# Performance work log

Hardware: AMD Instinct MI355X
Metric: run time of the kernel (lower is better)

## Reference

```python
import jax, jax.numpy as jnp
import numpy as np

N_HEADS = 8
WINDOW = 7

def _conv1x1(x, W, b):
    # x: [B,H,W,C]; 1x1 conv == per-pixel matmul
    return jnp.einsum('bhwc,cd->bhwd', x, W) + b

def _to_heads(t, nh):
    # [B,H,W,C] -> channels-first reshape [B, nh, C//nh, H*W] (matches tf transpose+reshape)
    B, H, W, C = t.shape
    return jnp.transpose(t, (0, 3, 1, 2)).reshape(B, nh, C // nh, H * W)

def setup_inputs() -> dict:
    key = jax.random.key(0)
    ks = jax.random.split(key, 8)
    B, H, W, C = 2, 56, 56, 256
    x = jax.random.normal(ks[0], (B, H, W, C), dtype=jnp.float32)
    s = 1.0 / np.sqrt(C)
    Wq = jax.random.normal(ks[1], (C, C), dtype=jnp.float32) * s
    bq = jnp.zeros((C,), dtype=jnp.float32)
    Wk = jax.random.normal(ks[2], (C, C), dtype=jnp.float32) * s
    bk = jnp.zeros((C,), dtype=jnp.float32)
    Wv = jax.random.normal(ks[3], (C, C), dtype=jnp.float32) * s
    bv = jnp.zeros((C,), dtype=jnp.float32)
    # original initializes gamma to 0 (output == x); use small nonzero so the
    # attention path is observable in outputs/grads
    gamma = jax.random.normal(ks[4], (1,), dtype=jnp.float32) * 0.1
    return {"x": x, "Wq": Wq, "bq": bq, "Wk": Wk, "bk": bk, "Wv": Wv, "bv": bv, "gamma": gamma}

def reference(x, Wq, bq, Wk, bk, Wv, bv, gamma):
    B, H, W, C = x.shape
    p = WINDOW // 2
    xp = jnp.pad(x, ((0, 0), (p, p), (p, p), (0, 0)), mode='reflect')  # [B,Hp,Wp,C]
    q = _to_heads(_conv1x1(x, Wq, bq), N_HEADS)    # [B,nh,dk,HW]
    k = _to_heads(_conv1x1(xp, Wk, bk), N_HEADS)   # [B,nh,dk,HpWp]
    v = _to_heads(_conv1x1(xp, Wv, bv), N_HEADS)   # [B,nh,dk,HpWp]
    energy = jnp.einsum('bhdq,bhdk->bhqk', q, k)   # [B,nh,HW,HpWp]
    attn = jax.nn.softmax(energy, axis=-1)
    out = jnp.einsum('bhdk,bhqk->bhdq', v, attn)   # [B,nh,dk,HW]
    out = out.reshape(B, C, H, W).transpose(0, 2, 3, 1)
    return gamma * out + x
```

## Files before the change

kernel.cpp:

```cpp
#include <hip/hip_runtime.h>

typedef unsigned short u16;
typedef float f32x4 __attribute__((ext_vector_type(4)));
typedef short bf16x8 __attribute__((ext_vector_type(8)));

__device__ __forceinline__ u16 f2bf(float f) {
    unsigned u = __float_as_uint(f);
    u = (u + 0x7FFFu + ((u >> 16) & 1u)) >> 16;
    return (u16)u;
}

#define LOG2E 1.4426950408889634f

#if __has_builtin(__builtin_amdgcn_exp2f)
__device__ __forceinline__ float exp2_fast(float x) { return __builtin_amdgcn_exp2f(x); }
#else
__device__ __forceinline__ float exp2_fast(float x) { return __expf(x * 0.6931471805599453f); }
#endif

__device__ __forceinline__ unsigned pack2bf(float a, float b) {
    unsigned ua = __float_as_uint(a) + 0x8000u;
    unsigned ub = __float_as_uint(b) + 0x8000u;
#if __has_builtin(__builtin_amdgcn_perm)
    return __builtin_amdgcn_perm(ub, ua, 0x07060302u);
#else
    return ((ua >> 16) & 0xFFFFu) | (ub & 0xFFFF0000u);
#endif
}

#if __has_builtin(__builtin_amdgcn_cvt_pk_bf16_f32)
typedef __bf16 bf2_t __attribute__((ext_vector_type(2)));
__device__ __forceinline__ unsigned cvtpk(float a, float b) {
    bf2_t r = __builtin_amdgcn_cvt_pk_bf16_f32(a, b);
    return __builtin_bit_cast(unsigned, r);
}
#else
__device__ __forceinline__ unsigned cvtpk(float a, float b) { return pack2bf(a, b); }
#endif

__device__ __forceinline__ bf16x8 bc8(uint4 u) { return __builtin_bit_cast(bf16x8, u); }

#if __has_builtin(__builtin_amdgcn_global_load_lds)
typedef const __attribute__((address_space(1))) void* as1cv;
typedef __attribute__((address_space(3))) void* as3v;
__device__ __forceinline__ void dma16(const void* g, void* lds_base, int lane) {
    __builtin_amdgcn_global_load_lds((as1cv)g, (as3v)lds_base, 16, 0, 0);
}
#else
__device__ __forceinline__ void dma16(const void* g, void* lds_base, int lane) {
    *(uint4*)((char*)lds_base + lane * 16) = *(const uint4*)g;
}
#endif

#define BB 2
#define HH 56
#define SQ 3136
#define CROWN 3584

#define WS_Q    0
#define WS_K    1605632
#define WS_V    3244032
#define WS_WT   4882432
#define WS_CB   5079040
#define WS_XB   5082624

__global__ __launch_bounds__(256) void prep_kernel(const float* __restrict__ x,
                                                   const float* __restrict__ Wq,
                                                   const float* __restrict__ Wk,
                                                   const float* __restrict__ Wv,
                                                   u16* __restrict__ wtf,
                                                   u16* __restrict__ kbf,
                                                   u16* __restrict__ vbf,
                                                   u16* __restrict__ crow,
                                                   u16* __restrict__ xbf) {
    __shared__ __align__(16) char SM[17408];
    int tid = threadIdx.x;
    int bid = blockIdx.x;

    if (bid < 48) {
        u16 (*T)[68] = (u16(*)[68])SM;
        int mode = bid >> 4, rem = bid & 15;
        int kx = (rem >> 2) * 64, dx = (rem & 3) * 64;
        const float* W = (mode == 0) ? Wq : ((mode == 1) ? Wk : Wv);
        float sc = (mode == 0) ? LOG2E : 1.0f;
        int r16 = tid >> 4, c4 = (tid & 15) * 4;
#pragma unroll
        for (int p = 0; p < 4; ++p) {
            int kr = p * 16 + r16;
            float4 f = *(const float4*)&W[(size_t)(kx + kr) * 256 + dx + c4];
            T[kr][c4 + 0] = f2bf(f.x * sc);
            T[kr][c4 + 1] = f2bf(f.y * sc);
            T[kr][c4 + 2] = f2bf(f.z * sc);
            T[kr][c4 + 3] = f2bf(f.w * sc);
        }
        __syncthreads();
        int l16 = tid & 15, nt_loc = (tid >> 4) & 3, quad = (tid >> 6) & 3;
#pragma unroll
        for (int s_loc = 0; s_loc < 2; ++s_loc) {
            int k0 = s_loc * 32 + quad * 8;
            int d_loc = nt_loc * 16 + l16;
            u16 tmp[8];
#pragma unroll
            for (int j = 0; j < 8; ++j) tmp[j] = T[k0 + j][d_loc];
            int d = dx + d_loc;
            int nz = d >> 7, ntg = (d >> 4) & 7;
            int s = (kx >> 5) + s_loc;
            int f = (nz * 8 + s) * 8 + ntg;
            int L = quad * 16 + l16;
            *(uint4*)&wtf[(size_t)mode * 65536 + (size_t)f * 512 + (size_t)L * 8] = *(uint4*)tmp;
        }
        uint4 z4 = (uint4){0, 0, 0, 0};
        if (mode == 0 && kx == 0 && dx == 0) {
            for (int i = tid; i < 4096; i += 256) {
                int bb = i >> 11, rem2 = i & 2047;
                int t = 196 + (rem2 >> 9), off = (rem2 & 511) * 8;
                *(uint4*)&kbf[(((size_t)(bb * 200 + t)) << 12) + off] = z4;
            }
        }
        if (mode == 1 && kx == 0 && dx == 0) {
            for (int i = tid; i < CROWN; i += 256) {
                u16 v = 0;
                if (i < SQ) {
                    int rr = i / 56, cc = i - rr * 56;
                    int mr = (((rr >= 1) && (rr <= 3)) || ((rr >= 52) && (rr <= 54))) ? 2 : 1;
                    int mc = (((cc >= 1) && (cc <= 3)) || ((cc >= 52) && (cc <= 54))) ? 2 : 1;
                    int prod = mr * mc;
                    v = (prod == 1) ? (u16)0x3F80 : ((prod == 2) ? (u16)0x4000 : (u16)0x4080);
                }
                crow[i] = v;
            }
        }
        if (mode == 2 && kx == 0 && dx == 0) {
            for (int i = tid; i < 4096; i += 256) {
                int bh = i >> 8, rem2 = i & 255;
                int rgp = 196 + (rem2 >> 6), off = (rem2 & 63) * 8;
                *(uint4*)&vbf[(((size_t)(bh * 200 + rgp)) << 9) + off] = z4;
            }
        }
    } else {
        float (*T)[256] = (float(*)[256])SM;
        int tile = bid - 48;
        int r = tid >> 4, c0 = (tid & 15) * 16;
        const float* src = x + ((size_t)tile * 16 + r) * 256 + c0;
#pragma unroll
        for (int k = 0; k < 4; ++k)
            *(float4*)&T[r][c0 + k * 4] = *(const float4*)&src[k * 4];
        __syncthreads();
#pragma unroll
        for (int e = 0; e < 2; ++e) {
            int g = tid + e * 256;
            int s = g >> 6, L = g & 63;
            const float* row = &T[L & 15][s * 32 + (L >> 4) * 8];
            uint4 pk = (uint4){pack2bf(row[0], row[1]), pack2bf(row[2], row[3]),
                               pack2bf(row[4], row[5]), pack2bf(row[6], row[7])};
            *(uint4*)&xbf[(size_t)tile * 4096 + (size_t)g * 8] = pk;
        }
    }
}

__global__ __launch_bounds__(256, 4) void proj_kernel(const u16* __restrict__ xbf,
                                                      const u16* __restrict__ wtf,
                                                      const float* __restrict__ bq,
                                                      const float* __restrict__ bk,
                                                      const float* __restrict__ bv,
                                                      u16* __restrict__ qbf,
                                                      u16* __restrict__ kbf,
                                                      u16* __restrict__ vbf) {
    int mode = blockIdx.y, nz = blockIdx.z;
    int mbase = blockIdx.x * 64;
    int tid = threadIdx.x;
    int wave = tid >> 6, lane = tid & 63, quad = (tid >> 4) & 3, l16 = tid & 15;
    const float* bias = (mode == 0) ? bq : ((mode == 1) ? bk : bv);
    float wsc = (mode == 0) ? LOG2E : 1.0f;
    const u16* wf = wtf + (size_t)mode * 65536 + (size_t)nz * 32768 + (size_t)lane * 8;
    const u16* xt = xbf + (((size_t)(mbase >> 4) + wave) << 12);

    f32x4 acc[8];
#pragma unroll
    for (int i = 0; i < 8; i++) acc[i] = (f32x4){0.f, 0.f, 0.f, 0.f};

#pragma unroll
    for (int s = 0; s < 8; ++s) {
        bf16x8 af = *(const bf16x8*)&xt[(s << 9) + lane * 8];
        if (mode == 2) {
#pragma unroll
            for (int nt = 0; nt < 8; nt++) {
                bf16x8 bfrag = *(const bf16x8*)&wf[(s * 8 + nt) * 512];
                acc[nt] = __builtin_amdgcn_mfma_f32_16x16x32_bf16(af, bfrag, acc[nt], 0, 0, 0);
            }
        } else {
#pragma unroll
            for (int nt = 0; nt < 8; nt++) {
                bf16x8 bfrag = *(const bf16x8*)&wf[(s * 8 + nt) * 512];
                acc[nt] = __builtin_amdgcn_mfma_f32_16x16x32_bf16(bfrag, af, acc[nt], 0, 0, 0);
            }
        }
    }

    if (mode == 2) {
        int b_ = (mbase >= SQ) ? 1 : 0;
        int kp0 = mbase - b_ * SQ + wave * 16 + quad * 4;
        int rg = (mbase - b_ * SQ + wave * 16) >> 4;
        float mult[4];
#pragma unroll
        for (int p = 0; p < 4; ++p) {
            int kp = kp0 + p;
            int rr = kp / 56, cc = kp - rr * 56;
            float mr = (((rr >= 1) && (rr <= 3)) || ((rr >= 52) && (rr <= 54))) ? 2.f : 1.f;
            float mc = (((cc >= 1) && (cc <= 3)) || ((cc >= 52) && (cc <= 54))) ? 2.f : 1.f;
            mult[p] = mr * mc;
        }
#pragma unroll
        for (int nt = 0; nt < 8; nt++) {
            int c = nz * 128 + nt * 16 + l16;
            float bvv = bias[c];
            int h_idx = nz * 4 + (nt >> 1);
            int L = (nt & 1) * 16 + l16 + ((quad >> 1) & 1) * 32;
            float va0 = (acc[nt][0] + bvv) * mult[0];
            float va1 = (acc[nt][1] + bvv) * mult[1];
            float va2 = (acc[nt][2] + bvv) * mult[2];
            float va3 = (acc[nt][3] + bvv) * mult[3];
            uint2 pk = (uint2){pack2bf(va0, va1), pack2bf(va2, va3)};
            *(uint2*)&vbf[(((size_t)((b_ * 8 + h_idx) * 200 + rg)) << 9) + L * 8 + (quad & 1) * 4] = pk;
        }
    } else {
        u16* outp = (mode == 0) ? qbf : kbf;
        int t = (mbase >> 4) + wave;
        int tt = (mode == 0) ? t : (t + (t >= 196 ? 4 : 0));
#pragma unroll
        for (int nt = 0; nt < 8; nt++) {
            int c0 = nz * 128 + nt * 16 + quad * 4;
            float4 b4 = *(const float4*)&bias[c0];
            float v0 = acc[nt][0] + b4.x * wsc;
            float v1 = acc[nt][1] + b4.y * wsc;
            float v2 = acc[nt][2] + b4.z * wsc;
            float v3 = acc[nt][3] + b4.w * wsc;
            int s_idx = nz * 4 + (nt >> 1);
            int Lrow = ((nt & 1) * 2 + (quad >> 1)) * 16 + l16;
            uint2 pk = (uint2){pack2bf(v0, v1), pack2bf(v2, v3)};
            *(uint2*)&outp[(((size_t)(tt * 8 + s_idx)) << 9) + Lrow * 8 + (quad & 1) * 4] = pk;
        }
    }
}

__global__ __launch_bounds__(256, 4) void attn_kernel(const u16* __restrict__ qb,
                                                      const u16* __restrict__ kb,
                                                      const u16* __restrict__ vtb,
                                                      const u16* __restrict__ crow,
                                                      const float* __restrict__ x,
                                                      const float* __restrict__ gammap,
                                                      float* __restrict__ out) {
    __shared__ __align__(16) u16 S[19968];

    int tid = threadIdx.x;
    int w = tid >> 6, lane = tid & 63, quad = lane >> 4, l16 = lane & 15;
    int bh = blockIdx.x;
    int b = bh >> 3, h = bh & 7;
    int qsub = blockIdx.y * 64;

    int qtile = b * 196 + blockIdx.y * 4;
    bf16x8 qf[4];
#pragma unroll
    for (int i = 0; i < 4; ++i)
        qf[i] = *(const bf16x8*)&qb[(((size_t)(qtile + i) * 8 + h) << 9) + lane * 8];

    const u16* kg = kb + ((size_t)(b * 200) << 12);
    const u16* vg = vtb + (((size_t)((b * 8 + h) * 200)) << 9);

    f32x4 o[4][2], lv[4];
#pragma unroll
    for (int i = 0; i < 4; ++i) {
        o[i][0] = (f32x4){0.f, 0.f, 0.f, 0.f};
        o[i][1] = (f32x4){0.f, 0.f, 0.f, 0.f};
        lv[i]   = (f32x4){0.f, 0.f, 0.f, 0.f};
    }

    int tA = w, tB = w + 4;
    auto stage = [&](int r_ch, int buf) {
        u16* base = &S[buf * 8192];
        int rgA = r_ch * 8 + tA, rgB = r_ch * 8 + tB;
        dma16(kg + (((size_t)rgA * 8 + h) << 9) + lane * 8, base + tA * 512, lane);
        dma16(kg + (((size_t)rgB * 8 + h) << 9) + lane * 8, base + tB * 512, lane);
        dma16(vg + (((size_t)rgA) << 9) + lane * 8, base + 4096 + tA * 512, lane);
        dma16(vg + (((size_t)rgB) << 9) + lane * 8, base + 4096 + tB * 512, lane);
    };

    int vOffA = tA * 512 + (((quad >> 1) * 32 + l16) << 3) + (quad & 1) * 4;
    int vOffB = tB * 512 + (((quad >> 1) * 32 + l16) << 3) + (quad & 1) * 4;

    auto round_body = [&](int r, int bR) {
        const u16* Kl = &S[bR * 8192];
        const u16* Vl = Kl + 4096;
        const u16* cnt = &S[16384] + r * 128;
        f32x4 z = (f32x4){0.f, 0.f, 0.f, 0.f};
        unsigned paw[4][4];

        {
            bf16x8 kfA = *(const bf16x8*)&Kl[tA * 512 + lane * 8];
            f32x4 eA[4];
            __builtin_amdgcn_s_setprio(1);
#pragma unroll
            for (int i = 0; i < 4; ++i)
                eA[i] = __builtin_amdgcn_mfma_f32_16x16x32_bf16(kfA, qf[i], z, 0, 0, 0);
            __builtin_amdgcn_s_setprio(0);
#pragma unroll
            for (int i = 0; i < 4; ++i) {
                paw[i][0] = cvtpk(exp2_fast(eA[i][0]), exp2_fast(eA[i][1]));
                paw[i][1] = cvtpk(exp2_fast(eA[i][2]), exp2_fast(eA[i][3]));
            }
        }
        {
            bf16x8 kfB = *(const bf16x8*)&Kl[tB * 512 + lane * 8];
            f32x4 eB[4];
            __builtin_amdgcn_s_setprio(1);
#pragma unroll
            for (int i = 0; i < 4; ++i)
                eB[i] = __builtin_amdgcn_mfma_f32_16x16x32_bf16(kfB, qf[i], z, 0, 0, 0);
            __builtin_amdgcn_s_setprio(0);
#pragma unroll
            for (int i = 0; i < 4; ++i) {
                paw[i][2] = cvtpk(exp2_fast(eB[i][0]), exp2_fast(eB[i][1]));
                paw[i][3] = cvtpk(exp2_fast(eB[i][2]), exp2_fast(eB[i][3]));
            }
        }
        uint2 ca = *(const uint2*)&cnt[tA * 16 + quad * 4];
        uint2 cc = *(const uint2*)&cnt[tB * 16 + quad * 4];
        bf16x8 cf = bc8((uint4){ca.x, ca.y, cc.x, cc.y});
        uint2 wA0 = *(const uint2*)&Vl[vOffA];
        uint2 wB0 = *(const uint2*)&Vl[vOffB];
        bf16x8 V0 = bc8((uint4){wA0.x, wA0.y, wB0.x, wB0.y});
        uint2 wA1 = *(const uint2*)&Vl[vOffA + 128];
        uint2 wB1 = *(const uint2*)&Vl[vOffB + 128];
        bf16x8 V1 = bc8((uint4){wA1.x, wA1.y, wB1.x, wB1.y});

        __builtin_amdgcn_s_setprio(1);
#pragma unroll
        for (int i = 0; i < 4; ++i) {
            bf16x8 pa = bc8((uint4){paw[i][0], paw[i][1], paw[i][2], paw[i][3]});
            o[i][0] = __builtin_amdgcn_mfma_f32_16x16x32_bf16(pa, V0, o[i][0], 0, 0, 0);
            o[i][1] = __builtin_amdgcn_mfma_f32_16x16x32_bf16(pa, V1, o[i][1], 0, 0, 0);
            lv[i]   = __builtin_amdgcn_mfma_f32_16x16x32_bf16(pa, cf, lv[i], 0, 0, 0);
        }
        __builtin_amdgcn_s_setprio(0);
    };

    {
        dma16(crow + w * 512 + lane * 8, (char*)&S[16384] + w * 1024, lane);
        if (w + 4 < 7)
            dma16(crow + (w + 4) * 512 + lane * 8, (char*)&S[16384] + (w + 4) * 1024, lane);
    }
    stage(0, 0);
    __syncthreads();

    for (int r = 0; r < 25; ++r) {
        if (r + 1 < 25) {
            stage(r + 1, (r + 1) & 1);
            asm volatile("s_waitcnt vmcnt(4)" ::: "memory");
        } else {
            asm volatile("s_waitcnt vmcnt(0)" ::: "memory");
        }
        round_body(r, r & 1);
    }
    __syncthreads();

    float* mg = (float*)&S[0];
    {
        int slot = ((w & 1) * 64 + lane) * 48;
        if (w >= 2) {
#pragma unroll
            for (int i = 0; i < 4; ++i) {
                *(f32x4*)&mg[slot + i * 8]      = o[i][0];
                *(f32x4*)&mg[slot + i * 8 + 4]  = o[i][1];
                *(f32x4*)&mg[slot + 32 + i * 4] = lv[i];
            }
        }
        __syncthreads();
        if (w < 2) {
#pragma unroll
            for (int i = 0; i < 4; ++i) {
                o[i][0] += *(const f32x4*)&mg[slot + i * 8];
                o[i][1] += *(const f32x4*)&mg[slot + i * 8 + 4];
                lv[i]   += *(const f32x4*)&mg[slot + 32 + i * 4];
            }
        }
        __syncthreads();
    }
    {
        int slot = lane * 48;
        if (w == 1) {
#pragma unroll
            for (int i = 0; i < 4; ++i) {
                *(f32x4*)&mg[slot + i * 8]      = o[i][0];
                *(f32x4*)&mg[slot + i * 8 + 4]  = o[i][1];
                *(f32x4*)&mg[slot + 32 + i * 4] = lv[i];
            }
        }
        __syncthreads();
        if (w == 0) {
            float gam = gammap[0];
#pragma unroll
            for (int i = 0; i < 4; ++i) {
                o[i][0] += *(const f32x4*)&mg[slot + i * 8];
                o[i][1] += *(const f32x4*)&mg[slot + i * 8 + 4];
                lv[i]   += *(const f32x4*)&mg[slot + 32 + i * 4];
#pragma unroll
                for (int r2 = 0; r2 < 4; ++r2) {
                    float scl = gam / lv[i][r2];
                    int q = qsub + i * 16 + quad * 4 + r2;
                    size_t base = ((size_t)(b * SQ + q) << 8) + h * 32 + l16;
                    out[base]      = o[i][0][r2] * scl + x[base];
                    out[base + 16] = o[i][1][r2] * scl + x[base + 16];
                }
            }
        }
    }
}

extern "C" void kernel_launch(void* const* d_in, const int* in_sizes, int n_in,
                              void* d_out, int out_size, void* d_ws, size_t ws_size,
                              hipStream_t stream) {
    const float* x     = (const float*)d_in[0];
    const float* Wq    = (const float*)d_in[1];
    const float* bq    = (const float*)d_in[2];
    const float* Wk    = (const float*)d_in[3];
    const float* bk    = (const float*)d_in[4];
    const float* Wv    = (const float*)d_in[5];
    const float* bv    = (const float*)d_in[6];
    const float* gamma = (const float*)d_in[7];
    float* out = (float*)d_out;

    u16* ws   = (u16*)d_ws;
    u16* qbf  = ws + WS_Q;
    u16* kbf  = ws + WS_K;
    u16* vbf  = ws + WS_V;
    u16* wtf  = ws + WS_WT;
    u16* crow = ws + WS_CB;
    u16* xbf  = ws + WS_XB;

    prep_kernel<<<440, 256, 0, stream>>>(x, Wq, Wk, Wv, wtf, kbf, vbf, crow, xbf);
    proj_kernel<<<dim3(98, 3, 2), 256, 0, stream>>>(xbf, wtf, bq, bk, bv, qbf, kbf, vbf);
    attn_kernel<<<dim3(16, 49), 256, 0, stream>>>(qbf, kbf, vbf, crow, x, gamma, out);
}
```

Before: 128.3 us.

## Software-pipeline QK and PV across rounds and repack V for vector LDS reads

Changes the V global layout so each wave reads its V fragments as full 16-byte LDS loads instead of gathering pairs of 8-byte pieces. It also restructures the attention main loop into a two-stage software pipeline: the QK+exp for the next round overlaps the PV MFMAs of the current round, with K and V staged separately under finer vmcnt waits. The aim is to hide exp and LDS latency behind MFMA work and cut LDS instruction count. It uses more registers for double-buffered probabilities, and the manual waitcnt and buffer indexing are fragile.

```diff
diff --git a/kernel.cpp b/kernel.cpp
--- a/kernel.cpp
+++ b/kernel.cpp
@@ -131,10 +131,13 @@
             }
         }
         if (mode == 2 && kx == 0 && dx == 0) {
-            for (int i = tid; i < 4096; i += 256) {
-                int bh = i >> 8, rem2 = i & 255;
-                int rgp = 196 + (rem2 >> 6), off = (rem2 & 63) * 8;
-                *(uint4*)&vbf[(((size_t)(bh * 200 + rgp)) << 9) + off] = z4;
+            for (int i = tid; i < 8192; i += 256) {
+                int bh = i >> 9, rem2 = i & 511;
+                int wp = rem2 >> 7, rem3 = rem2 & 127;
+                int vh = rem3 >> 6, ln = rem3 & 63;
+                size_t off = (size_t)bh * 102400 + (size_t)(96 + wp) * 1024
+                           + (size_t)vh * 512 + (size_t)ln * 8 + 4;
+                *(uint2*)&vbf[off] = (uint2){0, 0};
             }
         }
     } else {
@@ -201,6 +204,7 @@
         int b_ = (mbase >= SQ) ? 1 : 0;
         int kp0 = mbase - b_ * SQ + wave * 16 + quad * 4;
         int rg = (mbase - b_ * SQ + wave * 16) >> 4;
+        int ch = rg >> 3, wp = rg & 3, which = (rg >> 2) & 1;
         float mult[4];
 #pragma unroll
         for (int p = 0; p < 4; ++p) {
@@ -215,13 +219,15 @@
             int c = nz * 128 + nt * 16 + l16;
             float bvv = bias[c];
             int h_idx = nz * 4 + (nt >> 1);
-            int L = (nt & 1) * 16 + l16 + ((quad >> 1) & 1) * 32;
+            int bh2 = b_ * 8 + h_idx;
             float va0 = (acc[nt][0] + bvv) * mult[0];
             float va1 = (acc[nt][1] + bvv) * mult[1];
             float va2 = (acc[nt][2] + bvv) * mult[2];
             float va3 = (acc[nt][3] + bvv) * mult[3];
             uint2 pk = (uint2){pack2bf(va0, va1), pack2bf(va2, va3)};
-            *(uint2*)&vbf[(((size_t)((b_ * 8 + h_idx) * 200 + rg)) << 9) + L * 8 + (quad & 1) * 4] = pk;
+            size_t off = (size_t)bh2 * 102400 + (size_t)(ch * 4 + wp) * 1024
+                       + (size_t)(nt & 1) * 512 + (size_t)(quad * 16 + l16) * 8 + which * 4;
+            *(uint2*)&vbf[off] = pk;
         }
     } else {
         u16* outp = (mode == 0) ? qbf : kbf;
@@ -265,7 +271,7 @@
         qf[i] = *(const bf16x8*)&qb[(((size_t)(qtile + i) * 8 + h) << 9) + lane * 8];
 
     const u16* kg = kb + ((size_t)(b * 200) << 12);
-    const u16* vg = vtb + (((size_t)((b * 8 + h) * 200)) << 9);
+    const u16* vg = vtb + (size_t)bh * 102400;
 
     f32x4 o[4][2], lv[4];
 #pragma unroll
@@ -276,91 +282,99 @@
     }
 
     int tA = w, tB = w + 4;
-    auto stage = [&](int r_ch, int buf) {
+    int kOffA = tA * 512 + lane * 8;
+    int kOffB = tB * 512 + lane * 8;
+    int vOff0 = 4096 + w * 1024 + lane * 8;
+    int cOffA = tA * 16 + quad * 4;
+    int cOffB = tB * 16 + quad * 4;
+
+    const u16* kApt = kg + ((size_t)(tA * 8 + h) << 9);
+    const u16* kBpt = kg + ((size_t)(tB * 8 + h) << 9);
+    const u16* vpt  = vg + w * 1024;
+    const u16* cntp = &S[16384];
+
+    auto stageK = [&](int buf) {
         u16* base = &S[buf * 8192];
-        int rgA = r_ch * 8 + tA, rgB = r_ch * 8 + tB;
-        dma16(kg + (((size_t)rgA * 8 + h) << 9) + lane * 8, base + tA * 512, lane);
-        dma16(kg + (((size_t)rgB * 8 + h) << 9) + lane * 8, base + tB * 512, lane);
-        dma16(vg + (((size_t)rgA) << 9) + lane * 8, base + 4096 + tA * 512, lane);
-        dma16(vg + (((size_t)rgB) << 9) + lane * 8, base + 4096 + tB * 512, lane);
+        dma16(kApt + lane * 8, base + tA * 512, lane);
+        dma16(kBpt + lane * 8, base + tB * 512, lane);
+        kApt += 32768; kBpt += 32768;
     };
-
-    int vOffA = tA * 512 + (((quad >> 1) * 32 + l16) << 3) + (quad & 1) * 4;
-    int vOffB = tB * 512 + (((quad >> 1) * 32 + l16) << 3) + (quad & 1) * 4;
-
-    auto round_body = [&](int r, int bR) {
-        const u16* Kl = &S[bR * 8192];
-        const u16* Vl = Kl + 4096;
-        const u16* cnt = &S[16384] + r * 128;
+    auto stageV = [&](int buf) {
+        u16* base = &S[buf * 8192 + 4096 + w * 1024];
+        dma16(vpt + lane * 8, base, lane);
+        dma16(vpt + 512 + lane * 8, base + 512, lane);
+        vpt += 4096;
+    };
+
+    auto qk = [&](int bufK, unsigned (&po)[4][4]) {
+        const u16* Kl = &S[bufK * 8192];
         f32x4 z = (f32x4){0.f, 0.f, 0.f, 0.f};
-        unsigned paw[4][4];
-
-        {
-            bf16x8 kfA = *(const bf16x8*)&Kl[tA * 512 + lane * 8];
-            f32x4 eA[4];
-            __builtin_amdgcn_s_setprio(1);
-#pragma unroll
-            for (int i = 0; i < 4; ++i)
-                eA[i] = __builtin_amdgcn_mfma_f32_16x16x32_bf16(kfA, qf[i], z, 0, 0, 0);
-            __builtin_amdgcn_s_setprio(0);
-#pragma unroll
-            for (int i = 0; i < 4; ++i) {
-                paw[i][0] = cvtpk(exp2_fast(eA[i][0]), exp2_fast(eA[i][1]));
-                paw[i][1] = cvtpk(exp2_fast(eA[i][2]), exp2_fast(eA[i][3]));
-            }
-        }
-        {
-            bf16x8 kfB = *(const bf16x8*)&Kl[tB * 512 + lane * 8];
-            f32x4 eB[4];
-            __builtin_amdgcn_s_setprio(1);
-#pragma unroll
-            for (int i = 0; i < 4; ++i)
-                eB[i] = __builtin_amdgcn_mfma_f32_16x16x32_bf16(kfB, qf[i], z, 0, 0, 0);
-            __builtin_amdgcn_s_setprio(0);
-#pragma unroll
-            for (int i = 0; i < 4; ++i) {
-                paw[i][2] = cvtpk(exp2_fast(eB[i][0]), exp2_fast(eB[i][1]));
-                paw[i][3] = cvtpk(exp2_fast(eB[i][2]), exp2_fast(eB[i][3]));
-            }
-        }
-        uint2 ca = *(const uint2*)&cnt[tA * 16 + quad * 4];
-        uint2 cc = *(const uint2*)&cnt[tB * 16 + quad * 4];
-        bf16x8 cf = bc8((uint4){ca.x, ca.y, cc.x, cc.y});
-        uint2 wA0 = *(const uint2*)&Vl[vOffA];
-        uint2 wB0 = *(const uint2*)&Vl[vOffB];
-        bf16x8 V0 = bc8((uint4){wA0.x, wA0.y, wB0.x, wB0.y});
-        uint2 wA1 = *(const uint2*)&Vl[vOffA + 128];
-        uint2 wB1 = *(const uint2*)&Vl[vOffB + 128];
-        bf16x8 V1 = bc8((uint4){wA1.x, wA1.y, wB1.x, wB1.y});
-
+        bf16x8 kfA = *(const bf16x8*)&Kl[kOffA];
+        bf16x8 kfB = *(const bf16x8*)&Kl[kOffB];
+        f32x4 eA[4], eB[4];
         __builtin_amdgcn_s_setprio(1);
 #pragma unroll
+        for (int i = 0; i < 4; ++i)
+            eA[i] = __builtin_amdgcn_mfma_f32_16x16x32_bf16(kfA, qf[i], z, 0, 0, 0);
+#pragma unroll
+        for (int i = 0; i < 4; ++i)
+            eB[i] = __builtin_amdgcn_mfma_f32_16x16x32_bf16(kfB, qf[i], z, 0, 0, 0);
+        __builtin_amdgcn_s_setprio(0);
+#pragma unroll
         for (int i = 0; i < 4; ++i) {
-            bf16x8 pa = bc8((uint4){paw[i][0], paw[i][1], paw[i][2], paw[i][3]});
+            po[i][0] = cvtpk(exp2_fast(eA[i][0]), exp2_fast(eA[i][1]));
+            po[i][1] = cvtpk(exp2_fast(eA[i][2]), exp2_fast(eA[i][3]));
+            po[i][2] = cvtpk(exp2_fast(eB[i][0]), exp2_fast(eB[i][1]));
+            po[i][3] = cvtpk(exp2_fast(eB[i][2]), exp2_fast(eB[i][3]));
+        }
+    };
+
+    auto pv = [&](unsigned (&pc)[4][4], int bufS) {
+        const u16* Vl = &S[bufS * 8192];
+        bf16x8 V0 = *(const bf16x8*)&Vl[vOff0];
+        bf16x8 V1 = *(const bf16x8*)&Vl[vOff0 + 512];
+        uint2 ca = *(const uint2*)&cntp[cOffA];
+        uint2 cb2 = *(const uint2*)&cntp[cOffB];
+        bf16x8 cf = bc8((uint4){ca.x, ca.y, cb2.x, cb2.y});
+        __builtin_amdgcn_s_setprio(1);
+#pragma unroll
+        for (int i = 0; i < 4; ++i) {
+            bf16x8 pa = bc8((uint4){pc[i][0], pc[i][1], pc[i][2], pc[i][3]});
             o[i][0] = __builtin_amdgcn_mfma_f32_16x16x32_bf16(pa, V0, o[i][0], 0, 0, 0);
             o[i][1] = __builtin_amdgcn_mfma_f32_16x16x32_bf16(pa, V1, o[i][1], 0, 0, 0);
             lv[i]   = __builtin_amdgcn_mfma_f32_16x16x32_bf16(pa, cf, lv[i], 0, 0, 0);
         }
         __builtin_amdgcn_s_setprio(0);
+        cntp += 128;
     };
 
-    {
-        dma16(crow + w * 512 + lane * 8, (char*)&S[16384] + w * 1024, lane);
-        if (w + 4 < 7)
-            dma16(crow + (w + 4) * 512 + lane * 8, (char*)&S[16384] + (w + 4) * 1024, lane);
-    }
-    stage(0, 0);
+    dma16(crow + w * 512 + lane * 8, (char*)&S[16384] + w * 1024, lane);
+    if (w < 3)
+        dma16(crow + (w + 4) * 512 + lane * 8, (char*)&S[16384] + (w + 4) * 1024, lane);
+    stageK(0);
+    stageV(0);
+    stageK(1);
     __syncthreads();
 
-    for (int r = 0; r < 25; ++r) {
-        if (r + 1 < 25) {
-            stage(r + 1, (r + 1) & 1);
-            asm volatile("s_waitcnt vmcnt(4)" ::: "memory");
-        } else {
-            asm volatile("s_waitcnt vmcnt(0)" ::: "memory");
-        }
-        round_body(r, r & 1);
-    }
+    unsigned pa0[4][4], pa1[4][4];
+    qk(0, pa0);
+
+    auto iter = [&](unsigned (&pc)[4][4], unsigned (&pn)[4][4], int bufK1, int bufS) {
+        asm volatile("s_waitcnt vmcnt(2)" ::: "memory");
+        stageK(bufS);
+        stageV(bufK1);
+        qk(bufK1, pn);
+        asm volatile("s_waitcnt vmcnt(4)" ::: "memory");
+        pv(pc, bufS);
+    };
+
+    for (int r2 = 0; r2 < 12; ++r2) {
+        iter(pa0, pa1, 1, 0);
+        iter(pa1, pa0, 0, 1);
+    }
+    asm volatile("s_waitcnt vmcnt(0)" ::: "memory");
+    pv(pa0, 0);
+
     __syncthreads();
 
     float* mg = (float*)&S[0];
```

New measurement: 144.0 us. 12.3% more time.
